# Kernel optimization log

Hardware: AMD Instinct MI355X
Metric: run time of the kernel (lower is better)

Reference implementation:

```python
import jax, jax.numpy as jnp
import numpy as np

B, C, H, W, D = 2, 256, 16, 16, 16
HEADS, DIM_HEAD = 8, 64
HIDDEN = HEADS * DIM_HEAD  # 512
EPS = 1e-12  # torch F.normalize default eps


def setup_inputs() -> dict:
    key = jax.random.key(0)
    k1, k2, k3 = jax.random.split(key, 3)
    x = jax.random.normal(k1, (B, C, H, W, D), dtype=jnp.float32)
    g = jnp.ones((C,), dtype=jnp.float32)
    # conv 1x1 weights act as plain matrices over the channel dim
    w_qkv = jax.random.normal(k2, (3 * HIDDEN, C), dtype=jnp.float32) * (C ** -0.5)
    w_out = jax.random.normal(k3, (C, HIDDEN), dtype=jnp.float32) * (HIDDEN ** -0.5)
    b_out = jnp.zeros((C,), dtype=jnp.float32)
    return {"x": x, "g": g, "w_qkv": w_qkv, "w_out": w_out, "b_out": b_out}


def reference(x, g, w_qkv, w_out, b_out):
    b, c, h, w, d = x.shape
    n = h * w * d
    # RMSNorm3D: F.normalize(x, dim=1) * g * sqrt(C)
    norm = jnp.sqrt(jnp.sum(x * x, axis=1, keepdims=True))
    xn = x / jnp.maximum(norm, EPS) * g[None, :, None, None, None] * (c ** 0.5)
    xt = xn.reshape(b, c, n)  # [b, c, n]
    # 1x1 conv3d == channel matmul
    qkv = jnp.einsum('oc,bcn->bon', w_qkv, xt)  # [b, 3*hidden, n]
    q, k, v = jnp.split(qkv, 3, axis=1)
    def to_heads(t):  # [b, heads*dh, n] -> [b, heads, n, dh]
        return t.reshape(b, HEADS, DIM_HEAD, n).transpose(0, 1, 3, 2)
    q, k, v = to_heads(q), to_heads(k), to_heads(v)
    scale = DIM_HEAD ** -0.5
    sim = jnp.einsum('bhid,bhjd->bhij', q * scale, k)  # [b, heads, n, n]
    attn = jax.nn.softmax(sim, axis=-1)
    out = jnp.einsum('bhij,bhjd->bhid', attn, v)  # [b, heads, n, dh]
    out = out.transpose(0, 1, 3, 2).reshape(b, HIDDEN, n)  # [b, hidden, n]
    y = jnp.einsum('oc,bcn->bon', w_out, out) + b_out[None, :, None]
    return y.reshape(b, c, h, w, d)
```

## Files before the change

kernel.cpp:

```cpp
#include <hip/hip_runtime.h>
#include <type_traits>

#define DI __device__ __forceinline__

typedef __attribute__((ext_vector_type(8))) __bf16 vbf8;
typedef __attribute__((ext_vector_type(8))) short  vs8;
typedef __attribute__((ext_vector_type(4))) float  f4;
typedef __attribute__((ext_vector_type(4))) unsigned int u32x4;

static constexpr int BB   = 2;
static constexpr int C    = 256;
static constexpr int NN   = 4096;
static constexpr int HID  = 512;
static constexpr int QKVR = 1536;

static DI unsigned short f2bf(float f) {
  unsigned int u = __builtin_bit_cast(unsigned int, f);
  u += 0x7fffu + ((u >> 16) & 1u);
  return (unsigned short)(u >> 16);
}
static DI unsigned int cvtpk(float lo, float hi) {
  unsigned int r;
  asm("v_cvt_pk_bf16_f32 %0, %1, %2" : "=v"(r) : "v"(lo), "v"(hi));
  return r;
}
static DI float EXP2(float x) {
  float r;
  asm("v_exp_f32 %0, %1" : "=v"(r) : "v"(x));
  return r;
}
static DI float MAX3(float a, float b, float c) {
  float r;
  asm("v_max3_f32 %0, %1, %2, %3" : "=v"(r) : "v"(a), "v"(b), "v"(c));
  return r;
}
static DI void swap16(unsigned int &a, unsigned int &b) {
  asm("v_permlane16_swap_b32 %0, %1" : "+v"(a), "+v"(b));
}
static DI void swap32(unsigned int &a, unsigned int &b) {
  asm("v_permlane32_swap_b32 %0, %1" : "+v"(a), "+v"(b));
}

template <typename V>
static DI auto mfma_sel(V a, V b, f4 c, int)
    -> decltype(__builtin_amdgcn_mfma_f32_16x16x32_bf16(a, b, c, 0, 0, 0)) {
  return __builtin_amdgcn_mfma_f32_16x16x32_bf16(a, b, c, 0, 0, 0);
}
template <typename V>
static DI f4 mfma_sel(V a, V b, f4 c, long) {
  return __builtin_amdgcn_mfma_f32_16x16x32_bf16(
      __builtin_bit_cast(vs8, a), __builtin_bit_cast(vs8, b), c, 0, 0, 0);
}
static DI f4 MFMA(vs8 a, vs8 b, f4 c) {
  return mfma_sel(__builtin_bit_cast(vbf8, a), __builtin_bit_cast(vbf8, b), c, 0);
}

static DI void gll16(const unsigned short* g, unsigned short* l) {
  __builtin_amdgcn_global_load_lds(
      (const __attribute__((address_space(1))) unsigned int*)g,
      (__attribute__((address_space(3))) unsigned int*)l, 16, 0, 0);
}

__global__ void k_prep(const float* __restrict__ wqkv, const float* __restrict__ g,
                       const float* __restrict__ wout,
                       unsigned short* __restrict__ wg, unsigned short* __restrict__ wo) {
  int i = blockIdx.x * 256 + threadIdx.x;
  if (i < QKVR * C) wg[i] = f2bf(wqkv[i] * g[i & (C - 1)]);
  if (i < C * HID)  wo[i] = f2bf(wout[i]);
}

__global__ __launch_bounds__(256) void k_qkv(const float* __restrict__ x,
    const unsigned short* __restrict__ wg,
    unsigned short* __restrict__ qo, unsigned short* __restrict__ ko,
    unsigned short* __restrict__ vo) {
  __shared__ unsigned short xs[64 * 264];
  __shared__ float ps[4][64];
  __shared__ float inv[64];
  const int bo = blockIdx.x % 12;
  const int bn = (blockIdx.x / 12) & 63;
  const int b  = blockIdx.x / (12 * 64);
  const int o0 = bo * 128, n0 = bn * 64;
  const int tid = threadIdx.x;
  {
    const int nl = tid & 63, cb = tid >> 6;
    const float* xp = x + (size_t)b * C * NN + n0 + nl;
    float s = 0.f;
    #pragma unroll 4
    for (int kk = 0; kk < 64; ++kk) {
      int c = cb * 64 + kk;
      float v = xp[(size_t)c * NN];
      s += v * v;
      xs[nl * 264 + c] = f2bf(v);
    }
    ps[cb][nl] = s;
  }
  __syncthreads();
  if (tid < 64) {
    float t4 = ps[0][tid] + ps[1][tid] + ps[2][tid] + ps[3][tid];
    inv[tid] = 16.0f / fmaxf(sqrtf(t4), 1e-12f);
  }
  __syncthreads();
  const int wave = tid >> 6, lane = tid & 63, lr = lane & 15, lg = lane >> 4;
  const int orow = o0 + wave * 32;
  f4 acc[2][4] = { { {0,0,0,0},{0,0,0,0},{0,0,0,0},{0,0,0,0} },
                   { {0,0,0,0},{0,0,0,0},{0,0,0,0},{0,0,0,0} } };
  const unsigned short* wp0 = wg + (size_t)(orow + lr) * C + lg * 8;
  const unsigned short* wp1 = wg + (size_t)(orow + 16 + lr) * C + lg * 8;
  #pragma unroll
  for (int c0 = 0; c0 < C; c0 += 32) {
    vs8 af0 = *(const vs8*)(wp0 + c0);
    vs8 af1 = *(const vs8*)(wp1 + c0);
    #pragma unroll
    for (int nc = 0; nc < 4; ++nc) {
      vs8 bf = *(const vs8*)(&xs[(nc * 16 + lr) * 264 + c0 + lg * 8]);
      acc[0][nc] = MFMA(af0, bf, acc[0][nc]);
      acc[1][nc] = MFMA(af1, bf, acc[1][nc]);
    }
  }
  #pragma unroll
  for (int om = 0; om < 2; ++om) {
    const int om_row = orow + om * 16;
    const int otype = om_row >> 9;
    const int head  = (om_row >> 6) & 7;
    const int bh    = b * 8 + head;
    const int dbase = (om_row & 63) + lg * 4;
    #pragma unroll
    for (int nc = 0; nc < 4; ++nc) {
      const int n = n0 + nc * 16 + lr;
      float s = inv[nc * 16 + lr];
      if (otype == 0) s *= 0.125f * 1.44269504088896f;
      if (otype < 2) {
        unsigned short* dst = (otype == 0 ? qo : ko) + ((size_t)bh * NN + n) * 64 + dbase;
        unsigned long long pk = 0;
        #pragma unroll
        for (int r = 0; r < 4; ++r)
          pk |= (unsigned long long)f2bf(acc[om][nc][r] * s) << (16 * r);
        *(unsigned long long*)dst = pk;
      } else {
        #pragma unroll
        for (int r = 0; r < 4; ++r)
          vo[((size_t)bh * 64 + dbase + r) * NN + n] = f2bf(acc[om][nc][r] * s);
      }
    }
  }
}

__global__ __launch_bounds__(256) void k_attn(const unsigned short* __restrict__ qq,
    const unsigned short* __restrict__ kk, const unsigned short* __restrict__ vv,
    unsigned short* __restrict__ ob) {
  __shared__ unsigned short stg[2][8192];
  const int bid = blockIdx.x;
  const int swz = (bid & 7) * 64 + (bid >> 3);
  const int bh  = swz >> 5;
  const int qt  = swz & 31;
  const int tid = threadIdx.x, wave = tid >> 6, lane = tid & 63;
  const int lr = lane & 15, lg = lane >> 4;
  const int qbase = qt * 128 + wave * 32;
  const unsigned short* kb = kk + (size_t)bh * NN * 64;
  const unsigned short* vb = vv + (size_t)bh * 64 * NN;
  vs8 qf[2][2];
  #pragma unroll
  for (int qn = 0; qn < 2; ++qn)
    #pragma unroll
    for (int kd = 0; kd < 2; ++kd)
      qf[qn][kd] = *(const vs8*)(qq + ((size_t)bh * NN + qbase + qn * 16 + lr) * 64 + kd * 32 + lg * 8);
  const vs8 onesf = {0x3F80, 0x3F80, 0x3F80, 0x3F80, 0x3F80, 0x3F80, 0x3F80, 0x3F80};
  f4 oacc[4][2] = { { {0,0,0,0},{0,0,0,0} }, { {0,0,0,0},{0,0,0,0} },
                    { {0,0,0,0},{0,0,0,0} }, { {0,0,0,0},{0,0,0,0} } };
  f4 lacc[2] = { {0,0,0,0}, {0,0,0,0} };
  float m[2] = {0.f, 0.f};

  auto stage = [&](int j0, int buf) {
    #pragma unroll
    for (int p = 0; p < 2; ++p) {
      const int g  = wave * 2 + p;
      const int jt = g >> 1, kd = g & 1;
      gll16(kb + (size_t)(j0 + jt * 16 + lr) * 64 + kd * 32 + lg * 8,
            &stg[buf][g * 512]);
      const int dt = g >> 1, kj = g & 1;
      gll16(vb + (size_t)(dt * 16 + lr) * NN + j0 + kj * 32 + lg * 8,
            &stg[buf][4096 + g * 512]);
    }
  };

  stage(0, 0);
  asm volatile("s_waitcnt vmcnt(0)");
  __syncthreads();

  for (int t = 0; t < NN / 64; ++t) {
    const int cur = t & 1;
    if (t + 1 < NN / 64) stage((t + 1) * 64, cur ^ 1);
    const unsigned short* sbk = stg[cur];
    const unsigned short* sbv = stg[cur] + 4096;
    f4 s[4][2];
    #pragma unroll
    for (int jt = 0; jt < 4; ++jt)
      #pragma unroll
      for (int qn = 0; qn < 2; ++qn)
        s[jt][qn] = f4{-m[qn], -m[qn], -m[qn], -m[qn]};
    __builtin_amdgcn_s_setprio(1);
    #pragma unroll
    for (int jt = 0; jt < 4; ++jt) {
      vs8 k0 = *(const vs8*)(sbk + (jt * 2 + 0) * 512 + lane * 8);
      vs8 k1 = *(const vs8*)(sbk + (jt * 2 + 1) * 512 + lane * 8);
      #pragma unroll
      for (int qn = 0; qn < 2; ++qn) {
        s[jt][qn] = MFMA(k0, qf[qn][0], s[jt][qn]);
        s[jt][qn] = MFMA(k1, qf[qn][1], s[jt][qn]);
      }
    }
    __builtin_amdgcn_s_setprio(0);
    float pm[2];
    #pragma unroll
    for (int qn = 0; qn < 2; ++qn) {
      float t0 = MAX3(s[0][qn][0], s[0][qn][1], s[0][qn][2]);
      float t1 = MAX3(s[0][qn][3], s[1][qn][0], s[1][qn][1]);
      float t2 = MAX3(s[1][qn][2], s[1][qn][3], s[2][qn][0]);
      float t3 = MAX3(s[2][qn][1], s[2][qn][2], s[2][qn][3]);
      float t4 = MAX3(s[3][qn][0], s[3][qn][1], s[3][qn][2]);
      float t5 = MAX3(t0, t1, t2);
      float t6 = MAX3(t3, t4, s[3][qn][3]);
      pm[qn] = fmaxf(t5, t6);
    }
    if (!__all((pm[0] <= 8.f) & (pm[1] <= 8.f))) {
      #pragma unroll
      for (int qn = 0; qn < 2; ++qn) {
        float dm = pm[qn];
        dm = fmaxf(dm, __shfl_xor(dm, 16));
        dm = fmaxf(dm, __shfl_xor(dm, 32));
        dm = fmaxf(dm, 0.f);
        float a = EXP2(-dm);
        m[qn] += dm;
        #pragma unroll
        for (int mt = 0; mt < 4; ++mt)
          #pragma unroll
          for (int r = 0; r < 4; ++r)
            oacc[mt][qn][r] *= a;
        #pragma unroll
        for (int r = 0; r < 4; ++r) lacc[qn][r] *= a;
        #pragma unroll
        for (int jt = 0; jt < 4; ++jt)
          #pragma unroll
          for (int r = 0; r < 4; ++r)
            s[jt][qn][r] -= dm;
      }
    }
    unsigned int A[2][8];
    #pragma unroll
    for (int qn = 0; qn < 2; ++qn) {
      #pragma unroll
      for (int jt = 0; jt < 4; ++jt) {
        float p0 = EXP2(s[jt][qn][0]);
        float p1 = EXP2(s[jt][qn][1]);
        float p2 = EXP2(s[jt][qn][2]);
        float p3 = EXP2(s[jt][qn][3]);
        A[qn][2 * jt]     = cvtpk(p0, p1);
        A[qn][2 * jt + 1] = cvtpk(p2, p3);
      }
      swap32(A[qn][0], A[qn][2]); swap32(A[qn][1], A[qn][3]);
      swap16(A[qn][0], A[qn][2]); swap16(A[qn][1], A[qn][3]);
      swap32(A[qn][4], A[qn][6]); swap32(A[qn][5], A[qn][7]);
      swap16(A[qn][4], A[qn][6]); swap16(A[qn][5], A[qn][7]);
    }
    vs8 pb[2][2];
    #pragma unroll
    for (int qn = 0; qn < 2; ++qn) {
      pb[qn][0] = __builtin_bit_cast(vs8, u32x4{A[qn][0], A[qn][1], A[qn][2], A[qn][3]});
      pb[qn][1] = __builtin_bit_cast(vs8, u32x4{A[qn][4], A[qn][5], A[qn][6], A[qn][7]});
    }
    __builtin_amdgcn_s_setprio(1);
    #pragma unroll
    for (int kj = 0; kj < 2; ++kj) {
      #pragma unroll
      for (int mt = 0; mt < 4; ++mt) {
        vs8 vf = *(const vs8*)(sbv + (mt * 2 + kj) * 512 + lane * 8);
        oacc[mt][0] = MFMA(vf, pb[0][kj], oacc[mt][0]);
        oacc[mt][1] = MFMA(vf, pb[1][kj], oacc[mt][1]);
      }
      lacc[0] = MFMA(onesf, pb[0][kj], lacc[0]);
      lacc[1] = MFMA(onesf, pb[1][kj], lacc[1]);
    }
    __builtin_amdgcn_s_setprio(0);
    asm volatile("s_waitcnt vmcnt(0)");
    __syncthreads();
  }
  const int b = bh >> 3, h = bh & 7;
  float rl[2] = {1.0f / lacc[0][0], 1.0f / lacc[1][0]};
  #pragma unroll
  for (int mt = 0; mt < 4; ++mt)
    #pragma unroll
    for (int qn = 0; qn < 2; ++qn)
      #pragma unroll
      for (int r = 0; r < 4; ++r) {
        int d = mt * 16 + lg * 4 + r;
        int q = qbase + qn * 16 + lr;
        ob[((size_t)(b * HID + h * 64 + d)) * NN + q] = f2bf(oacc[mt][qn][r] * rl[qn]);
      }
}

__global__ __launch_bounds__(256) void k_out(const unsigned short* __restrict__ obuf,
    const unsigned short* __restrict__ wo, const float* __restrict__ bout,
    float* __restrict__ y) {
  __shared__ unsigned short os[64 * 136];
  const int bo = blockIdx.x & 3;
  const int bn = (blockIdx.x >> 2) & 63;
  const int b  = blockIdx.x >> 8;
  const int o0 = bo * 64, n0 = bn * 64;
  const int tid = threadIdx.x, wave = tid >> 6, lane = tid & 63, lr = lane & 15, lg = lane >> 4;
  const int orow = o0 + wave * 16;
  f4 acc[4] = { {0,0,0,0},{0,0,0,0},{0,0,0,0},{0,0,0,0} };
  for (int c0 = 0; c0 < HID; c0 += 128) {
    __syncthreads();
    {
      const int nl = tid & 63, cb = tid >> 6;
      const unsigned short* sp = obuf + ((size_t)b * HID + c0) * NN + n0 + nl;
      #pragma unroll 4
      for (int t = 0; t < 32; ++t) {
        int cc = cb * 32 + t;
        os[nl * 136 + cc] = sp[(size_t)cc * NN];
      }
    }
    __syncthreads();
    const unsigned short* wp = wo + (size_t)(orow + lr) * HID + c0 + lg * 8;
    #pragma unroll
    for (int cc0 = 0; cc0 < 128; cc0 += 32) {
      vs8 af = *(const vs8*)(wp + cc0);
      #pragma unroll
      for (int nc = 0; nc < 4; ++nc) {
        vs8 bf = *(const vs8*)(&os[(nc * 16 + lr) * 136 + cc0 + lg * 8]);
        acc[nc] = MFMA(af, bf, acc[nc]);
      }
    }
  }
  #pragma unroll
  for (int nc = 0; nc < 4; ++nc) {
    const int n = n0 + nc * 16 + lr;
    #pragma unroll
    for (int r = 0; r < 4; ++r)
      y[((size_t)b * C + orow + lg * 4 + r) * NN + n] = acc[nc][r] + bout[orow + lg * 4 + r];
  }
}

extern "C" void kernel_launch(void* const* d_in, const int* in_sizes, int n_in,
                              void* d_out, int out_size, void* d_ws, size_t ws_size,
                              hipStream_t stream) {
  const float* x    = (const float*)d_in[0];
  const float* g    = (const float*)d_in[1];
  const float* wqkv = (const float*)d_in[2];
  const float* wout = (const float*)d_in[3];
  const float* bout = (const float*)d_in[4];
  float* y = (float*)d_out;
  char* ws = (char*)d_ws;
  unsigned short* wg  = (unsigned short*)(ws);
  unsigned short* wo  = (unsigned short*)(ws + 786432);
  unsigned short* qb  = (unsigned short*)(ws + 1048576);
  unsigned short* kb  = (unsigned short*)(ws + 1048576 + 8388608);
  unsigned short* vtb = (unsigned short*)(ws + 1048576 + 2 * 8388608);
  unsigned short* ob  = (unsigned short*)(ws + 1048576 + 3 * 8388608);
  k_prep<<<1536, 256, 0, stream>>>(wqkv, g, wout, wg, wo);
  k_qkv<<<1536, 256, 0, stream>>>(x, wg, qb, kb, vtb);
  k_attn<<<512, 256, 0, stream>>>(qb, kb, vtb, ob);
  k_out<<<512, 256, 0, stream>>>(ob, wo, bout, y);
}
```

Measured before the change: 148.9 us.

## Software-pipeline QK^T of next tile with softmax/PV of current tile using triple-buffered LDS

Moves the attention loop to a three-buffer LDS ring and computes the QK^T scores for tile t+1 before the softmax and PV of tile t. This lets the QK and PV MFMA chains overlap with the exp/max work of the neighbouring tile, and it prefetches K/V two tiles ahead. When the running max is rescaled, the scores already computed for the next tile are shifted too, so results stay correct. The cost is more LDS (48KB per block) and an extra set of score registers, which may lower occupancy.

```diff
diff --git a/kernel.cpp b/kernel.cpp
--- a/kernel.cpp
+++ b/kernel.cpp
@@ -148,7 +148,7 @@
 __global__ __launch_bounds__(256) void k_attn(const unsigned short* __restrict__ qq,
     const unsigned short* __restrict__ kk, const unsigned short* __restrict__ vv,
     unsigned short* __restrict__ ob) {
-  __shared__ unsigned short stg[2][8192];
+  __shared__ unsigned short stg[3][8192];
   const int bid = blockIdx.x;
   const int swz = (bid & 7) * 64 + (bid >> 3);
   const int bh  = swz >> 5;
@@ -169,6 +169,7 @@
                     { {0,0,0,0},{0,0,0,0} }, { {0,0,0,0},{0,0,0,0} } };
   f4 lacc[2] = { {0,0,0,0}, {0,0,0,0} };
   float m[2] = {0.f, 0.f};
+  f4 sA[4][2], sB[4][2];
 
   auto stage = [&](int j0, int buf) {
     #pragma unroll
@@ -183,107 +184,116 @@
     }
   };
 
+#define QK(S, BN)                                                              \
+  {                                                                            \
+    _Pragma("unroll") for (int jt = 0; jt < 4; ++jt) {                         \
+      S[jt][0] = f4{-m[0], -m[0], -m[0], -m[0]};                               \
+      S[jt][1] = f4{-m[1], -m[1], -m[1], -m[1]};                               \
+      vs8 k0 = *(const vs8*)(stg[BN] + (jt * 2 + 0) * 512 + lane * 8);         \
+      vs8 k1 = *(const vs8*)(stg[BN] + (jt * 2 + 1) * 512 + lane * 8);         \
+      S[jt][0] = MFMA(k0, qf[0][0], S[jt][0]);                                 \
+      S[jt][0] = MFMA(k1, qf[0][1], S[jt][0]);                                 \
+      S[jt][1] = MFMA(k0, qf[1][0], S[jt][1]);                                 \
+      S[jt][1] = MFMA(k1, qf[1][1], S[jt][1]);                                 \
+    }                                                                          \
+  }
+
+#define SMPV(SC, SN, BC, HASN)                                                 \
+  {                                                                            \
+    float pm[2];                                                               \
+    _Pragma("unroll") for (int qn = 0; qn < 2; ++qn) {                         \
+      float t0 = MAX3(SC[0][qn][0], SC[0][qn][1], SC[0][qn][2]);               \
+      float t1 = MAX3(SC[0][qn][3], SC[1][qn][0], SC[1][qn][1]);               \
+      float t2 = MAX3(SC[1][qn][2], SC[1][qn][3], SC[2][qn][0]);               \
+      float t3 = MAX3(SC[2][qn][1], SC[2][qn][2], SC[2][qn][3]);               \
+      float t4 = MAX3(SC[3][qn][0], SC[3][qn][1], SC[3][qn][2]);               \
+      pm[qn] = fmaxf(MAX3(t0, t1, t2), MAX3(t3, t4, SC[3][qn][3]));            \
+    }                                                                          \
+    if (!__all((pm[0] <= 8.f) & (pm[1] <= 8.f))) {                             \
+      _Pragma("unroll") for (int qn = 0; qn < 2; ++qn) {                       \
+        float dm = pm[qn];                                                     \
+        dm = fmaxf(dm, __shfl_xor(dm, 16));                                    \
+        dm = fmaxf(dm, __shfl_xor(dm, 32));                                    \
+        dm = fmaxf(dm, 0.f);                                                   \
+        float a = EXP2(-dm);                                                   \
+        m[qn] += dm;                                                           \
+        _Pragma("unroll") for (int mt = 0; mt < 4; ++mt)                       \
+          _Pragma("unroll") for (int r = 0; r < 4; ++r)                        \
+            oacc[mt][qn][r] *= a;                                              \
+        _Pragma("unroll") for (int r = 0; r < 4; ++r) lacc[qn][r] *= a;        \
+        _Pragma("unroll") for (int jt = 0; jt < 4; ++jt)                       \
+          _Pragma("unroll") for (int r = 0; r < 4; ++r) {                      \
+            SC[jt][qn][r] -= dm;                                               \
+            if (HASN) SN[jt][qn][r] -= dm;                                     \
+          }                                                                    \
+      }                                                                        \
+    }                                                                          \
+    unsigned int A[2][8];                                                      \
+    _Pragma("unroll") for (int qn = 0; qn < 2; ++qn) {                         \
+      _Pragma("unroll") for (int jt = 0; jt < 4; ++jt) {                       \
+        float p0 = EXP2(SC[jt][qn][0]);                                        \
+        float p1 = EXP2(SC[jt][qn][1]);                                        \
+        float p2 = EXP2(SC[jt][qn][2]);                                        \
+        float p3 = EXP2(SC[jt][qn][3]);                                        \
+        A[qn][2 * jt]     = cvtpk(p0, p1);                                     \
+        A[qn][2 * jt + 1] = cvtpk(p2, p3);                                     \
+      }                                                                        \
+      swap32(A[qn][0], A[qn][2]); swap32(A[qn][1], A[qn][3]);                  \
+      swap16(A[qn][0], A[qn][2]); swap16(A[qn][1], A[qn][3]);                  \
+      swap32(A[qn][4], A[qn][6]); swap32(A[qn][5], A[qn][7]);                  \
+      swap16(A[qn][4], A[qn][6]); swap16(A[qn][5], A[qn][7]);                  \
+    }                                                                          \
+    vs8 pb0[2], pb1[2];                                                        \
+    pb0[0] = __builtin_bit_cast(vs8, u32x4{A[0][0], A[0][1], A[0][2], A[0][3]});\
+    pb0[1] = __builtin_bit_cast(vs8, u32x4{A[0][4], A[0][5], A[0][6], A[0][7]});\
+    pb1[0] = __builtin_bit_cast(vs8, u32x4{A[1][0], A[1][1], A[1][2], A[1][3]});\
+    pb1[1] = __builtin_bit_cast(vs8, u32x4{A[1][4], A[1][5], A[1][6], A[1][7]});\
+    __builtin_amdgcn_s_setprio(1);                                             \
+    _Pragma("unroll") for (int kj = 0; kj < 2; ++kj) {                         \
+      _Pragma("unroll") for (int mt = 0; mt < 4; ++mt) {                       \
+        vs8 vf = *(const vs8*)(stg[BC] + 4096 + (mt * 2 + kj) * 512 + lane * 8);\
+        oacc[mt][0] = MFMA(vf, pb0[kj], oacc[mt][0]);                          \
+        oacc[mt][1] = MFMA(vf, pb1[kj], oacc[mt][1]);                          \
+      }                                                                        \
+      lacc[0] = MFMA(onesf, pb0[kj], lacc[0]);                                 \
+      lacc[1] = MFMA(onesf, pb1[kj], lacc[1]);                                 \
+    }                                                                          \
+    __builtin_amdgcn_s_setprio(0);                                             \
+  }
+
+#define ITER(T, SC, SN, BC, BN, BS, DO_STAGE, DO_QK)                           \
+  {                                                                            \
+    if (DO_STAGE) stage((T + 2) * 64, BS);                                     \
+    if (DO_QK) QK(SN, BN);                                                     \
+    SMPV(SC, SN, BC, DO_QK);                                                   \
+    asm volatile("s_waitcnt vmcnt(0)");                                        \
+    __syncthreads();                                                           \
+  }
+
   stage(0, 0);
+  stage(64, 1);
   asm volatile("s_waitcnt vmcnt(0)");
   __syncthreads();
-
-  for (int t = 0; t < NN / 64; ++t) {
-    const int cur = t & 1;
-    if (t + 1 < NN / 64) stage((t + 1) * 64, cur ^ 1);
-    const unsigned short* sbk = stg[cur];
-    const unsigned short* sbv = stg[cur] + 4096;
-    f4 s[4][2];
-    #pragma unroll
-    for (int jt = 0; jt < 4; ++jt)
-      #pragma unroll
-      for (int qn = 0; qn < 2; ++qn)
-        s[jt][qn] = f4{-m[qn], -m[qn], -m[qn], -m[qn]};
-    __builtin_amdgcn_s_setprio(1);
-    #pragma unroll
-    for (int jt = 0; jt < 4; ++jt) {
-      vs8 k0 = *(const vs8*)(sbk + (jt * 2 + 0) * 512 + lane * 8);
-      vs8 k1 = *(const vs8*)(sbk + (jt * 2 + 1) * 512 + lane * 8);
-      #pragma unroll
-      for (int qn = 0; qn < 2; ++qn) {
-        s[jt][qn] = MFMA(k0, qf[qn][0], s[jt][qn]);
-        s[jt][qn] = MFMA(k1, qf[qn][1], s[jt][qn]);
-      }
-    }
-    __builtin_amdgcn_s_setprio(0);
-    float pm[2];
-    #pragma unroll
-    for (int qn = 0; qn < 2; ++qn) {
-      float t0 = MAX3(s[0][qn][0], s[0][qn][1], s[0][qn][2]);
-      float t1 = MAX3(s[0][qn][3], s[1][qn][0], s[1][qn][1]);
-      float t2 = MAX3(s[1][qn][2], s[1][qn][3], s[2][qn][0]);
-      float t3 = MAX3(s[2][qn][1], s[2][qn][2], s[2][qn][3]);
-      float t4 = MAX3(s[3][qn][0], s[3][qn][1], s[3][qn][2]);
-      float t5 = MAX3(t0, t1, t2);
-      float t6 = MAX3(t3, t4, s[3][qn][3]);
-      pm[qn] = fmaxf(t5, t6);
-    }
-    if (!__all((pm[0] <= 8.f) & (pm[1] <= 8.f))) {
-      #pragma unroll
-      for (int qn = 0; qn < 2; ++qn) {
-        float dm = pm[qn];
-        dm = fmaxf(dm, __shfl_xor(dm, 16));
-        dm = fmaxf(dm, __shfl_xor(dm, 32));
-        dm = fmaxf(dm, 0.f);
-        float a = EXP2(-dm);
-        m[qn] += dm;
-        #pragma unroll
-        for (int mt = 0; mt < 4; ++mt)
-          #pragma unroll
-          for (int r = 0; r < 4; ++r)
-            oacc[mt][qn][r] *= a;
-        #pragma unroll
-        for (int r = 0; r < 4; ++r) lacc[qn][r] *= a;
-        #pragma unroll
-        for (int jt = 0; jt < 4; ++jt)
-          #pragma unroll
-          for (int r = 0; r < 4; ++r)
-            s[jt][qn][r] -= dm;
-      }
-    }
-    unsigned int A[2][8];
-    #pragma unroll
-    for (int qn = 0; qn < 2; ++qn) {
-      #pragma unroll
-      for (int jt = 0; jt < 4; ++jt) {
-        float p0 = EXP2(s[jt][qn][0]);
-        float p1 = EXP2(s[jt][qn][1]);
-        float p2 = EXP2(s[jt][qn][2]);
-        float p3 = EXP2(s[jt][qn][3]);
-        A[qn][2 * jt]     = cvtpk(p0, p1);
-        A[qn][2 * jt + 1] = cvtpk(p2, p3);
-      }
-      swap32(A[qn][0], A[qn][2]); swap32(A[qn][1], A[qn][3]);
-      swap16(A[qn][0], A[qn][2]); swap16(A[qn][1], A[qn][3]);
-      swap32(A[qn][4], A[qn][6]); swap32(A[qn][5], A[qn][7]);
-      swap16(A[qn][4], A[qn][6]); swap16(A[qn][5], A[qn][7]);
-    }
-    vs8 pb[2][2];
-    #pragma unroll
-    for (int qn = 0; qn < 2; ++qn) {
-      pb[qn][0] = __builtin_bit_cast(vs8, u32x4{A[qn][0], A[qn][1], A[qn][2], A[qn][3]});
-      pb[qn][1] = __builtin_bit_cast(vs8, u32x4{A[qn][4], A[qn][5], A[qn][6], A[qn][7]});
-    }
-    __builtin_amdgcn_s_setprio(1);
-    #pragma unroll
-    for (int kj = 0; kj < 2; ++kj) {
-      #pragma unroll
-      for (int mt = 0; mt < 4; ++mt) {
-        vs8 vf = *(const vs8*)(sbv + (mt * 2 + kj) * 512 + lane * 8);
-        oacc[mt][0] = MFMA(vf, pb[0][kj], oacc[mt][0]);
-        oacc[mt][1] = MFMA(vf, pb[1][kj], oacc[mt][1]);
-      }
-      lacc[0] = MFMA(onesf, pb[0][kj], lacc[0]);
-      lacc[1] = MFMA(onesf, pb[1][kj], lacc[1]);
-    }
-    __builtin_amdgcn_s_setprio(0);
-    asm volatile("s_waitcnt vmcnt(0)");
-    __syncthreads();
-  }
+  QK(sA, 0);
+
+  for (int i = 0; i < 10; ++i) {
+    const int t = i * 6;
+    ITER(t + 0, sA, sB, 0, 1, 2, true, true);
+    ITER(t + 1, sB, sA, 1, 2, 0, true, true);
+    ITER(t + 2, sA, sB, 2, 0, 1, true, true);
+    ITER(t + 3, sB, sA, 0, 1, 2, true, true);
+    ITER(t + 4, sA, sB, 1, 2, 0, true, true);
+    ITER(t + 5, sB, sA, 2, 0, 1, true, true);
+  }
+  ITER(60, sA, sB, 0, 1, 2, true,  true);
+  ITER(61, sB, sA, 1, 2, 0, true,  true);
+  ITER(62, sA, sB, 2, 0, 1, false, true);
+  ITER(63, sB, sA, 0, 1, 2, false, false);
+
+#undef ITER
+#undef SMPV
+#undef QK
+
   const int b = bh >> 3, h = bh & 7;
   float rl[2] = {1.0f / lacc[0][0], 1.0f / lacc[1][0]};
   #pragma unroll
```

Result: slower. 173.3 us (+16.4%).
